# Performance work log

Measured on AMD Instinct MI355X. Metric: run time of the kernel, lower is better.

Reference implementation:

```python
import jax, jax.numpy as jnp
import numpy as np
from jax import lax

EPS_BN = 1e-5
SMOOTH = 1e-5


def conv3x3(x, w):
    # x: [N,C,H,W], w: [O,I,3,3], stride 1, padding 1 (SAME)
    return lax.conv_general_dilated(
        x, w, window_strides=(1, 1), padding='SAME',
        dimension_numbers=('NCHW', 'OIHW', 'NCHW'))


def batchnorm(x, gamma, beta):
    # training-mode BatchNorm2d: batch statistics over (N,H,W), biased var
    mean = jnp.mean(x, axis=(0, 2, 3), keepdims=True)
    var = jnp.mean(jnp.square(x - mean), axis=(0, 2, 3), keepdims=True)
    g = gamma.reshape(1, -1, 1, 1)
    b = beta.reshape(1, -1, 1, 1)
    return (x - mean) * lax.rsqrt(var + EPS_BN) * g + b


def tanimoto(a, b, axes):
    tpl = jnp.sum(a * b, axis=axes, keepdims=True)
    sq = jnp.sum(a * a + b * b, axis=axes, keepdims=True)
    return (tpl + SMOOTH) / (sq - tpl + SMOOTH)


def tanimoto_compl(a, b, axes):
    return 0.5 * (tanimoto(a, b, axes) + tanimoto(1.0 - a, 1.0 - b, axes))


def setup_inputs() -> dict:
    key = jax.random.key(0)
    ks = jax.random.split(key, 5)
    N, Cin, Cout, H, W = 8, 64, 64, 256, 256
    x = jax.random.normal(ks[0], (N, Cin, H, W), dtype=jnp.float32)
    fan = Cin * 9
    wq = jax.random.normal(ks[1], (Cout, Cin, 3, 3), dtype=jnp.float32) / np.sqrt(fan)
    wk = jax.random.normal(ks[2], (Cout, Cin, 3, 3), dtype=jnp.float32) / np.sqrt(fan)
    wv = jax.random.normal(ks[3], (Cout, Cin, 3, 3), dtype=jnp.float32) / np.sqrt(fan)
    ones = jnp.ones((Cout,), dtype=jnp.float32)
    zeros = jnp.zeros((Cout,), dtype=jnp.float32)
    return {
        'x': x,
        'wq': wq, 'gq': ones, 'bq': zeros,
        'wk': wk, 'gk': ones, 'bk': zeros,
        'wv': wv, 'gv': ones, 'bv': zeros,
        'g_norm': ones, 'b_norm': zeros,
    }


def reference(x, wq, gq, bq, wk, gk, bk, wv, gv, bv, g_norm, b_norm):
    q = jax.nn.sigmoid(batchnorm(conv3x3(x, wq), gq, bq))
    k = jax.nn.sigmoid(batchnorm(conv3x3(x, wk), gk, bk))
    v = jax.nn.sigmoid(batchnorm(conv3x3(x, wv), gv, bv))
    attn_spatial = tanimoto_compl(q, k, axes=(1,))      # [N,1,H,W]
    attn_channel = tanimoto_compl(q, k, axes=(2, 3))    # [N,C,1,1]
    attention = 0.5 * (attn_spatial * v + attn_channel * v)
    return batchnorm(attention, g_norm, b_norm)
```

## Files before the change

### kernel.cpp

```cpp
#include <hip/hip_runtime.h>

typedef unsigned short u16;
typedef __attribute__((ext_vector_type(8))) short short8;
typedef __attribute__((ext_vector_type(4))) float f32x4;

#define OFF_SUMS 0ul
#define OFF_WT   26624ul
#define OFF_ASP  247808ul
#define OFF_CONV 2344960ul
#define S_SUM   0
#define S_SSQ   768
#define S_SC    1536
#define S_BI    1728
#define M_A1    1920
#define M_A23   2432
#define M_A45   2944
#define M_V1    3456
#define M_V2    3968
#define M_AV    4480
#define M_AV2   4992
#define M_A2V2  5504
#define S_ACH   6016
#define S_SCA   6528
#define S_BIA   6592
#define S_NFLOAT 6656

__device__ __forceinline__ float bf2f(u16 v) {
  union { unsigned u; float f; } x; x.u = ((unsigned)v) << 16; return x.f;
}
__device__ __forceinline__ u16 f2bf(float f) {
  union { float f; unsigned u; } x; x.f = f;
  unsigned r = x.u + 0x7fffu + ((x.u >> 16) & 1u);
  return (u16)(r >> 16);
}
__device__ __forceinline__ float frcp(float x) { return __builtin_amdgcn_rcpf(x); }
__device__ __forceinline__ float sigmoidf_(float x) { return frcp(1.f + __expf(-x)); }

template <int CTRL, int RMASK>
__device__ __forceinline__ float dpp_add(float x) {
  int m = __builtin_amdgcn_update_dpp(0, __builtin_bit_cast(int, x), CTRL, RMASK, 0xf, true);
  return x + __builtin_bit_cast(float, m);
}
__device__ __forceinline__ float wsum64(float x) {
  x = dpp_add<0x111, 0xf>(x);
  x = dpp_add<0x112, 0xf>(x);
  x = dpp_add<0x114, 0xf>(x);
  x = dpp_add<0x118, 0xf>(x);
  x = dpp_add<0x142, 0xa>(x);
  x = dpp_add<0x143, 0xc>(x);
  return __builtin_bit_cast(float, __builtin_amdgcn_readlane(__builtin_bit_cast(int, x), 63));
}

__global__ void transpose_k(const float* __restrict__ x, u16* __restrict__ xt) {
  __shared__ u16 t[64][130];
  const int bid = blockIdx.x;
  const int wtile = bid & 1, h = (bid >> 1) & 255, n = bid >> 9;
  const int w0 = wtile << 7;
  const int tid = threadIdx.x;
  for (int i = tid; i < 8192; i += 256) {
    int c = i >> 7, w = i & 127;
    t[c][w] = f2bf(x[(((n << 6) + c) << 16) + (h << 8) + w0 + w]);
  }
  __syncthreads();
  for (int i = tid; i < 8192; i += 256) {
    int w = i >> 6, c = i & 63;
    xt[(long)((((n << 8) + h) << 8) + w0 + w) * 64 + c] = t[c][w];
  }
}

__global__ void repack_k(const float* __restrict__ wq, const float* __restrict__ wk,
                         const float* __restrict__ wv, u16* __restrict__ wt) {
  int i = blockIdx.x * 256 + threadIdx.x;
  if (i >= 110592) return;
  int conv = i / 36864, j = i % 36864;
  int oc = j / 576, r2 = j % 576, c = r2 / 9, dd = r2 % 9;
  const float* src = conv == 0 ? wq : (conv == 1 ? wk : wv);
  wt[(dd * 192 + conv * 64 + oc) * 64 + c] = f2bf(src[j]);
}

__global__ __launch_bounds__(256, 2) void conv_k(const u16* __restrict__ xt,
                                                 const u16* __restrict__ wt,
                                                 u16* __restrict__ conv,
                                                 float* __restrict__ S) {
  __shared__ u16 lx[3 * 8320];
  const int bid = blockIdx.x;
  const int wtile = bid & 1, h = (bid >> 1) & 255, n = bid >> 9;
  const int w0 = wtile << 7;
  const int tid = threadIdx.x;
  for (int g = tid; g < 3120; g += 256) {
    int row = g / 1040;
    int r2 = g - row * 1040;
    int w = r2 >> 3, cg = r2 & 7;
    int hs = h + row - 1, wsr = w0 + w - 1;
    uint4 val = make_uint4(0u, 0u, 0u, 0u);
    if ((unsigned)hs < 256u && (unsigned)wsr < 256u)
      val = *(const uint4*)(xt + (long)((((n << 8) + hs) << 8) + wsr) * 64 + (cg << 3));
    int idx = ((w << 6) + (cg << 3)) ^ ((w & 7) << 3);
    *(uint4*)(&lx[row * 8320 + idx]) = val;
  }
  __syncthreads();
  const int lane = tid & 63, wave = tid >> 6;
  const int quad = lane >> 4, l15 = lane & 15;
  f32x4 acc[3][8];
#pragma unroll
  for (int a = 0; a < 3; ++a)
#pragma unroll
    for (int b = 0; b < 8; ++b) acc[a][b] = (f32x4){0.f, 0.f, 0.f, 0.f};

#pragma unroll
  for (int dy = 0; dy < 3; ++dy) {
#pragma unroll
    for (int dx = 0; dx < 3; ++dx) {
      const u16* wp = wt + (dy * 3 + dx) * 12288;
      short8 bfr[3][2];
#pragma unroll
      for (int nt = 0; nt < 3; ++nt)
#pragma unroll
        for (int kc = 0; kc < 2; ++kc)
          bfr[nt][kc] = *(const short8*)(wp + ((wave * 3 + nt) * 16 + l15) * 64 + kc * 32 + quad * 8);
#pragma unroll
      for (int kc = 0; kc < 2; ++kc) {
        short8 afr[8];
#pragma unroll
        for (int mt = 0; mt < 8; ++mt) {
          const int wloc = mt * 16 + l15 + dx;
          int idx = ((wloc << 6) + (kc << 5) + (quad << 3)) ^ ((wloc & 7) << 3);
          afr[mt] = *(const short8*)(&lx[dy * 8320 + idx]);
        }
#pragma unroll
        for (int mt = 0; mt < 8; ++mt)
#pragma unroll
          for (int nt = 0; nt < 3; ++nt)
            acc[nt][mt] = __builtin_amdgcn_mfma_f32_16x16x32_bf16(afr[mt], bfr[nt][kc], acc[nt][mt], 0, 0, 0);
      }
    }
  }
  const long pix0 = (long)bid * 128;
#pragma unroll
  for (int nt = 0; nt < 3; ++nt) {
    const int oc = (wave * 3 + nt) * 16 + l15;
#pragma unroll
    for (int mt = 0; mt < 8; ++mt) {
      const long pr = pix0 + mt * 16 + quad * 4;
#pragma unroll
      for (int r = 0; r < 4; ++r)
        conv[(pr + r) * 192 + oc] = f2bf(acc[nt][mt][r]);
    }
  }
  const int sh = (bid & 3) * 192;
#pragma unroll
  for (int nt = 0; nt < 3; ++nt) {
    float s = 0.f, ss = 0.f;
#pragma unroll
    for (int mt = 0; mt < 8; ++mt)
#pragma unroll
      for (int r = 0; r < 4; ++r) {
        float x = acc[nt][mt][r];
        s += x; ss += x * x;
      }
    s += __shfl_xor(s, 16); ss += __shfl_xor(ss, 16);
    s += __shfl_xor(s, 32); ss += __shfl_xor(ss, 32);
    if (lane < 16) {
      const int oc = (wave * 3 + nt) * 16 + l15;
      atomicAdd(&S[S_SUM + sh + oc], s);
      atomicAdd(&S[S_SSQ + sh + oc], ss);
    }
  }
}

__global__ void bnparam_k(float* __restrict__ S, const float* gq, const float* bq, const float* gk,
                          const float* bk, const float* gv, const float* bv) {
  int t = threadIdx.x;
  int cv = t >> 6, c = t & 63;
  float g = cv == 0 ? gq[c] : (cv == 1 ? gk[c] : gv[c]);
  float b = cv == 0 ? bq[c] : (cv == 1 ? bk[c] : bv[c]);
  float sm = 0.f, sq = 0.f;
#pragma unroll
  for (int sh = 0; sh < 4; ++sh) { sm += S[S_SUM + sh * 192 + t]; sq += S[S_SSQ + sh * 192 + t]; }
  const float inv = 1.f / 524288.f;
  float mean = sm * inv;
  float var = sq * inv - mean * mean;
  float rstd = rsqrtf(var + 1e-5f);
  float sc = g * rstd;
  S[S_SC + t] = sc;
  S[S_BI + t] = b - mean * sc;
}

__global__ void k3_k(const u16* __restrict__ conv, float* __restrict__ S, float* __restrict__ asp) {
  __shared__ float red[4][8][64];
  const int tid = threadIdx.x, lane = tid & 63, wave = tid >> 6;
  const int bid = blockIdx.x;
  const int n = bid >> 9;
  const long p0 = (long)bid * 128 + wave * 32;
  const float sq = S[S_SC + lane], bq = S[S_BI + lane];
  const float sk = S[S_SC + 64 + lane], bk = S[S_BI + 64 + lane];
  const float sv = S[S_SC + 128 + lane], bv = S[S_BI + 128 + lane];
  float A1 = 0.f, A23 = 0.f, A45 = 0.f, V1 = 0.f, V2 = 0.f, AV = 0.f, AV2 = 0.f, A2V2 = 0.f;
  float myasp = 0.f;
#pragma unroll 4
  for (int i = 0; i < 32; ++i) {
    const u16* row = conv + (p0 + i) * 192;
    float q = sigmoidf_(bf2f(row[lane]) * sq + bq);
    float k = sigmoidf_(bf2f(row[64 + lane]) * sk + bk);
    float v = sigmoidf_(bf2f(row[128 + lane]) * sv + bv);
    float p1 = q * k, p23 = q * q + k * k, p45 = q + k;
    A1 += p1; A23 += p23; A45 += p45;
    float s1 = wsum64(p1);
    float s23 = wsum64(p23);
    float s45 = wsum64(p45);
    const float sm = 1e-5f;
    float t1 = (s1 + sm) * frcp(s23 - s1 + sm);
    float t2 = (64.f - s45 + s1 + sm) * frcp(64.f - s45 + s23 - s1 + sm);
    float a = 0.5f * (t1 + t2);
    if (i == (lane & 31)) myasp = a;
    float av = a * v;
    V1 += v; V2 += v * v; AV += av; AV2 += av * v; A2V2 += av * av;
  }
  if (lane < 32) asp[p0 + lane] = myasp;
  red[wave][0][lane] = A1;  red[wave][1][lane] = A23; red[wave][2][lane] = A45;
  red[wave][3][lane] = V1;  red[wave][4][lane] = V2;  red[wave][5][lane] = AV;
  red[wave][6][lane] = AV2; red[wave][7][lane] = A2V2;
  __syncthreads();
  if (tid < 64) {
    const int mb[8] = {M_A1, M_A23, M_A45, M_V1, M_V2, M_AV, M_AV2, M_A2V2};
#pragma unroll
    for (int m = 0; m < 8; ++m) {
      float t = red[0][m][tid] + red[1][m][tid] + red[2][m][tid] + red[3][m][tid];
      atomicAdd(&S[mb[m] + n * 64 + tid], t);
    }
  }
}

__global__ void k4_k(float* __restrict__ S, const float* gn, const float* bn_) {
  __shared__ float r1[512], r2[512];
  const int t = threadIdx.x;
  float A1 = S[M_A1 + t], A23 = S[M_A23 + t], A45 = S[M_A45 + t];
  const float sm = 1e-5f, cnt = 65536.f;
  float t1 = (A1 + sm) / (A23 - A1 + sm);
  float t2 = (cnt - A45 + A1 + sm) / (cnt - A45 + A23 - A1 + sm);
  float ach = 0.5f * (t1 + t2);
  S[S_ACH + t] = ach;
  r1[t] = 0.5f * (S[M_AV + t] + ach * S[M_V1 + t]);
  r2[t] = 0.25f * (S[M_A2V2 + t] + 2.f * ach * S[M_AV2 + t] + ach * ach * S[M_V2 + t]);
  __syncthreads();
  if (t < 64) {
    float s = 0.f, ss = 0.f;
#pragma unroll
    for (int n = 0; n < 8; ++n) { s += r1[n * 64 + t]; ss += r2[n * 64 + t]; }
    const float inv = 1.f / 524288.f;
    float mean = s * inv;
    float var = ss * inv - mean * mean;
    float rstd = rsqrtf(var + 1e-5f);
    float sc = gn[t] * rstd;
    S[S_SCA + t] = sc;
    S[S_BIA + t] = bn_[t] - mean * sc;
  }
}

__global__ void k6_k(const u16* __restrict__ conv, const float* __restrict__ S,
                     const float* __restrict__ asp, float* __restrict__ out) {
  __shared__ float t[128][65];
  const int tid = threadIdx.x, lane = tid & 63, wave = tid >> 6;
  const int n = blockIdx.x >> 9;
  const int hw0 = (blockIdx.x & 511) << 7;
  const long P0 = (long)blockIdx.x * 128;
  const float sv = S[S_SC + 128 + lane], bv = S[S_BI + 128 + lane];
  const float av = S[S_ACH + n * 64 + lane];
  const float sA = S[S_SCA + lane], bA = S[S_BIA + lane];
  for (int i = wave; i < 128; i += 4) {
    const long p = P0 + i;
    float v = sigmoidf_(bf2f(conv[p * 192 + 128 + lane]) * sv + bv);
    float att = 0.5f * (asp[p] + av) * v;
    t[i][lane] = att * sA + bA;
  }
  __syncthreads();
  const int c = tid >> 2, sub = tid & 3;
  const long plane = ((long)((n << 6) + c)) << 16;
  for (int i = 0; i < 8; ++i) {
    const int pst = (i * 4 + sub) << 2;
    f32x4 vbuf;
#pragma unroll
    for (int j = 0; j < 4; ++j) vbuf[j] = t[pst + j][c];
    *(f32x4*)(&out[plane + hw0 + pst]) = vbuf;
  }
}

extern "C" void kernel_launch(void* const* d_in, const int* in_sizes, int n_in,
                              void* d_out, int out_size, void* d_ws, size_t ws_size,
                              hipStream_t stream) {
  (void)in_sizes; (void)n_in; (void)out_size; (void)ws_size;
  const float* x  = (const float*)d_in[0];
  const float* wq = (const float*)d_in[1];
  const float* gq = (const float*)d_in[2];
  const float* bq = (const float*)d_in[3];
  const float* wk = (const float*)d_in[4];
  const float* gk = (const float*)d_in[5];
  const float* bk = (const float*)d_in[6];
  const float* wv = (const float*)d_in[7];
  const float* gv = (const float*)d_in[8];
  const float* bv = (const float*)d_in[9];
  const float* gn = (const float*)d_in[10];
  const float* bn_ = (const float*)d_in[11];
  char* ws = (char*)d_ws;
  float* S   = (float*)(ws + OFF_SUMS);
  u16* wt    = (u16*)(ws + OFF_WT);
  float* asp = (float*)(ws + OFF_ASP);
  u16* conv  = (u16*)(ws + OFF_CONV);
  float* out = (float*)d_out;
  u16* xt  = (u16*)d_out;

  (void)hipMemsetAsync(S, 0, S_NFLOAT * 4, stream);
  transpose_k<<<4096, 256, 0, stream>>>(x, xt);
  repack_k<<<432, 256, 0, stream>>>(wq, wk, wv, wt);
  conv_k<<<4096, 256, 0, stream>>>(xt, wt, conv, S);
  bnparam_k<<<1, 192, 0, stream>>>(S, gq, bq, gk, bk, gv, bv);
  k3_k<<<4096, 256, 0, stream>>>(conv, S, asp);
  k4_k<<<1, 512, 0, stream>>>(S, gn, bn_);
  k6_k<<<4096, 256, 0, stream>>>(conv, S, asp, out);
}
```

Measured before the change: 587.2 us.

## Switch conv MFMA to 32x32x16 tiles with 2x2 wave layout and prepacked weights

The conv kernel moves from 16x16x32 to 32x32x16 bf16 MFMA, splitting the block's waves 2x2 over pixels and output channels. Each MFMA now does more work per issued instruction and fewer LDS A-fragment reads are needed per FLOP. The weight repack is rewritten so each lane's B fragment is one contiguous 16-byte load. This changes the output store pattern and the accumulator register layout, which may affect register pressure and occupancy.

```diff
diff --git a/kernel.cpp b/kernel.cpp
--- a/kernel.cpp
+++ b/kernel.cpp
@@ -3,6 +3,7 @@
 typedef unsigned short u16;
 typedef __attribute__((ext_vector_type(8))) short short8;
 typedef __attribute__((ext_vector_type(4))) float f32x4;
+typedef __attribute__((ext_vector_type(16))) float f32x16;
 
 #define OFF_SUMS 0ul
 #define OFF_WT   26624ul
@@ -72,10 +73,14 @@
                          const float* __restrict__ wv, u16* __restrict__ wt) {
   int i = blockIdx.x * 256 + threadIdx.x;
   if (i >= 110592) return;
-  int conv = i / 36864, j = i % 36864;
-  int oc = j / 576, r2 = j % 576, c = r2 / 9, dd = r2 % 9;
-  const float* src = conv == 0 ? wq : (conv == 1 ? wk : wv);
-  wt[(dd * 192 + conv * 64 + oc) * 64 + c] = f2bf(src[j]);
+  int j = i & 7, l = (i >> 3) & 63, kc = (i >> 9) & 3;
+  int t2 = i >> 11;
+  int ocg = t2 % 6, dydx = t2 / 6;
+  int oc = ocg * 32 + (l & 31);
+  int ch = kc * 16 + (l >> 5) * 8 + j;
+  int cs = oc >> 6, ol = oc & 63;
+  const float* src = cs == 0 ? wq : (cs == 1 ? wk : wv);
+  wt[i] = f2bf(src[(ol * 64 + ch) * 9 + dydx]);
 }
 
 __global__ __launch_bounds__(256, 2) void conv_k(const u16* __restrict__ xt,
@@ -100,51 +105,59 @@
   }
   __syncthreads();
   const int lane = tid & 63, wave = tid >> 6;
-  const int quad = lane >> 4, l15 = lane & 15;
-  f32x4 acc[3][8];
+  const int l31 = lane & 31, half = lane >> 5;
+  const int wm = wave & 1, wn = wave >> 1;
+  f32x16 acc[3][2];
 #pragma unroll
   for (int a = 0; a < 3; ++a)
 #pragma unroll
-    for (int b = 0; b < 8; ++b) acc[a][b] = (f32x4){0.f, 0.f, 0.f, 0.f};
+    for (int b = 0; b < 2; ++b)
+#pragma unroll
+      for (int e = 0; e < 16; ++e) acc[a][b][e] = 0.f;
 
 #pragma unroll
   for (int dy = 0; dy < 3; ++dy) {
 #pragma unroll
     for (int dx = 0; dx < 3; ++dx) {
       const u16* wp = wt + (dy * 3 + dx) * 12288;
-      short8 bfr[3][2];
+      short8 bfr[3][4];
 #pragma unroll
       for (int nt = 0; nt < 3; ++nt)
 #pragma unroll
-        for (int kc = 0; kc < 2; ++kc)
-          bfr[nt][kc] = *(const short8*)(wp + ((wave * 3 + nt) * 16 + l15) * 64 + kc * 32 + quad * 8);
-#pragma unroll
-      for (int kc = 0; kc < 2; ++kc) {
-        short8 afr[8];
-#pragma unroll
-        for (int mt = 0; mt < 8; ++mt) {
-          const int wloc = mt * 16 + l15 + dx;
-          int idx = ((wloc << 6) + (kc << 5) + (quad << 3)) ^ ((wloc & 7) << 3);
+        for (int kc = 0; kc < 4; ++kc)
+          bfr[nt][kc] = *(const short8*)(wp + ((wn * 3 + nt) * 4 + kc) * 512 + lane * 8);
+#pragma unroll
+      for (int kc = 0; kc < 4; ++kc) {
+        short8 afr[2];
+#pragma unroll
+        for (int mt = 0; mt < 2; ++mt) {
+          const int px = wm * 64 + mt * 32 + l31 + dx;
+          const int chb = kc * 16 + half * 8;
+          int idx = ((px << 6) + chb) ^ ((px & 7) << 3);
           afr[mt] = *(const short8*)(&lx[dy * 8320 + idx]);
         }
 #pragma unroll
-        for (int mt = 0; mt < 8; ++mt)
+        for (int mt = 0; mt < 2; ++mt)
 #pragma unroll
           for (int nt = 0; nt < 3; ++nt)
-            acc[nt][mt] = __builtin_amdgcn_mfma_f32_16x16x32_bf16(afr[mt], bfr[nt][kc], acc[nt][mt], 0, 0, 0);
+            acc[nt][mt] = __builtin_amdgcn_mfma_f32_32x32x16_bf16(afr[mt], bfr[nt][kc], acc[nt][mt], 0, 0, 0);
       }
     }
   }
-  const long pix0 = (long)bid * 128;
+  const long pix0 = (long)bid * 128 + wm * 64;
 #pragma unroll
   for (int nt = 0; nt < 3; ++nt) {
-    const int oc = (wave * 3 + nt) * 16 + l15;
-#pragma unroll
-    for (int mt = 0; mt < 8; ++mt) {
-      const long pr = pix0 + mt * 16 + quad * 4;
-#pragma unroll
-      for (int r = 0; r < 4; ++r)
-        conv[(pr + r) * 192 + oc] = f2bf(acc[nt][mt][r]);
+    const int oc = wn * 96 + nt * 32 + l31;
+#pragma unroll
+    for (int mt = 0; mt < 2; ++mt) {
+      const long pxb = pix0 + mt * 32 + half * 4;
+#pragma unroll
+      for (int rq = 0; rq < 4; ++rq)
+#pragma unroll
+        for (int rr = 0; rr < 4; ++rr) {
+          const long px = pxb + rr + 8 * rq;
+          conv[px * 192 + oc] = f2bf(acc[nt][mt][rq * 4 + rr]);
+        }
     }
   }
   const int sh = (bid & 3) * 192;
@@ -152,16 +165,15 @@
   for (int nt = 0; nt < 3; ++nt) {
     float s = 0.f, ss = 0.f;
 #pragma unroll
-    for (int mt = 0; mt < 8; ++mt)
-#pragma unroll
-      for (int r = 0; r < 4; ++r) {
+    for (int mt = 0; mt < 2; ++mt)
+#pragma unroll
+      for (int r = 0; r < 16; ++r) {
         float x = acc[nt][mt][r];
         s += x; ss += x * x;
       }
-    s += __shfl_xor(s, 16); ss += __shfl_xor(ss, 16);
     s += __shfl_xor(s, 32); ss += __shfl_xor(ss, 32);
-    if (lane < 16) {
-      const int oc = (wave * 3 + nt) * 16 + l15;
+    if (lane < 32) {
+      const int oc = wn * 96 + nt * 32 + lane;
       atomicAdd(&S[S_SUM + sh + oc], s);
       atomicAdd(&S[S_SSQ + sh + oc], ss);
     }
```

Measured after the change: 552.6 us. 5.9% less time.
